# Optimization experiments

Measured on AMD Instinct MI355X. Metric: run time of the kernel, lower is better.

## Reference

```python
import jax, jax.numpy as jnp
import numpy as np

E = 1024
H = 16
CH = E // H

def setup_inputs() -> dict:
    key = jax.random.key(0)
    ks = jax.random.split(key, 9)
    s = E ** -0.5
    return {
        'x': jax.random.normal(ks[0], (4, 2048, E), dtype=jnp.float32),
        'Wq': jax.random.normal(ks[1], (E, E), dtype=jnp.float32) * s,
        'bq': jnp.zeros((E,), dtype=jnp.float32),
        'Wk': jax.random.normal(ks[2], (E, E), dtype=jnp.float32) * s,
        'bk': jnp.zeros((E,), dtype=jnp.float32),
        'Wv': jax.random.normal(ks[3], (E, E), dtype=jnp.float32) * s,
        'bv': jnp.zeros((E,), dtype=jnp.float32),
        'Wo': jax.random.normal(ks[4], (E, E), dtype=jnp.float32) * s,
        'bo': jnp.zeros((E,), dtype=jnp.float32),
    }

def _split_heads(t):
    # [..., n, H*ch] -> [..., H, n, ch]
    b, n, e = t.shape
    return t.reshape(b, n, H, CH).transpose(0, 2, 1, 3)

def reference(x, Wq, bq, Wk, bk, Wv, bv, Wo, bo):
    scale = CH ** -0.5
    q = _split_heads(x @ Wq.T + bq)  # [b,H,n,ch]
    k = _split_heads(x @ Wk.T + bk)
    v = _split_heads(x @ Wv.T + bv)
    att = jnp.einsum('bhqc,bhkc->bhqk', q, k) * scale
    att = jax.nn.softmax(att, axis=-1)
    out = jnp.einsum('bhqk,bhkc->bhqc', att, v)  # [b,H,n,ch]
    b, h, n, c = out.shape
    out = out.transpose(0, 2, 1, 3).reshape(b, n, h * c)
    return out @ Wo.T + bo
```

## Files before the change

### kernel.cpp

```cpp
#include <hip/hip_runtime.h>
#include <stdint.h>

#define EMB   1024
#define NHEAD 16
#define CHD   64
#define NB    4
#define SEQ   2048
#define NTOK  (NB * SEQ)
#define KDIM  1024

typedef __attribute__((ext_vector_type(8))) short  bf16x8;
typedef __attribute__((ext_vector_type(4))) short  short4v;
typedef __attribute__((ext_vector_type(4))) float  f32x4;
typedef __attribute__((ext_vector_type(4))) float  float4v;

__device__ __forceinline__ short f2bf(float f) {
    unsigned int u = __float_as_uint(f);
    u += 0x7fffu + ((u >> 16) & 1u);
    return (short)(u >> 16);
}

__device__ __forceinline__ void async16(const short* g, short* l) {
    __builtin_amdgcn_global_load_lds((__attribute__((address_space(1))) void const*)g,
                                     (__attribute__((address_space(3))) void*)l, 16, 0, 0);
}

__global__ __launch_bounds__(256) void cvt_all(const float* __restrict__ x,
                                               const float* __restrict__ Wq,
                                               const float* __restrict__ Wk,
                                               const float* __restrict__ Wv,
                                               const float* __restrict__ Wo,
                                               short* __restrict__ xb,
                                               short* __restrict__ Wqb,
                                               short* __restrict__ Wkb,
                                               short* __restrict__ Wvb,
                                               short* __restrict__ Wob) {
    int bid = blockIdx.x;
    const float* src;
    short* dst;
    int idx;
    if (bid < 8192) {
        src = x; dst = xb; idx = bid * 256 + threadIdx.x;
    } else {
        int w  = (bid - 8192) >> 10;
        int lb = (bid - 8192) & 1023;
        src = (w == 0) ? Wq : (w == 1) ? Wk : (w == 2) ? Wv : Wo;
        dst = (w == 0) ? Wqb : (w == 1) ? Wkb : (w == 2) ? Wvb : Wob;
        idx = lb * 256 + threadIdx.x;
    }
    float4v v = ((const float4v*)src)[idx];
    short4v s;
    s.x = f2bf(v.x); s.y = f2bf(v.y); s.z = f2bf(v.z); s.w = f2bf(v.w);
    ((short4v*)dst)[idx] = s;
}

__device__ __forceinline__ void gemm_core(const short* __restrict__ Atile,
                                          const short* __restrict__ Btile,
                                          short* As, short* Bs, f32x4 acc[4][4]) {
    const int tid  = threadIdx.x;
    const int wave = tid >> 6, lane = tid & 63;
    const int quad = lane >> 4, l16 = lane & 15;
    const int wm = (wave >> 1) * 64, wn = (wave & 1) * 64;
    const int srow = lane >> 2;
    const int scol = (lane & 3) * 8;

    for (int k0 = 0; k0 < KDIM; k0 += 32) {
        __syncthreads();
#pragma unroll
        for (int c = 0; c < 2; ++c) {
            int chunk = wave * 2 + c;
            int row = chunk * 16 + srow;
            async16(Atile + (size_t)row * KDIM + k0 + scol, As + chunk * 512);
            async16(Btile + (size_t)row * KDIM + k0 + scol, Bs + chunk * 512);
        }
        __syncthreads();
        bf16x8 af[4], bfr[4];
#pragma unroll
        for (int i = 0; i < 4; ++i)
            af[i] = *(const bf16x8*)&As[(wm + i * 16 + l16) * 32 + quad * 8];
#pragma unroll
        for (int j = 0; j < 4; ++j)
            bfr[j] = *(const bf16x8*)&Bs[(wn + j * 16 + l16) * 32 + quad * 8];
#pragma unroll
        for (int i = 0; i < 4; ++i)
#pragma unroll
            for (int j = 0; j < 4; ++j)
                acc[i][j] = __builtin_amdgcn_mfma_f32_16x16x32_bf16(af[i], bfr[j], acc[i][j], 0, 0, 0);
    }
}

#define QSCALE 0.1803368801111204f


#define MFMA16(A,B,C) __builtin_amdgcn_mfma_f32_16x16x32_bf16(A,B,C,0,0,0)
#define BARR  { __builtin_amdgcn_s_barrier(); __builtin_amdgcn_sched_barrier(0); }
#define VMC4  asm volatile("s_waitcnt vmcnt(4)" ::: "memory");
#define VMC0  asm volatile("s_waitcnt vmcnt(0)" ::: "memory");
#define PRIO1 __builtin_amdgcn_s_setprio(1);
#define PRIO0 __builtin_amdgcn_s_setprio(0);

#define STAGE_A_(BUF,H,T) { \
    async16(aS0 + (size_t)(H)*131072 + (T)*64, sm + (BUF)*32768 + (H)*8192 + stA); \
    async16(aS1 + (size_t)(H)*131072 + (T)*64, sm + (BUF)*32768 + (H)*8192 + 4096 + stA); }
#define STAGE_B_(BUF,H,T) { \
    async16(bS0 + (size_t)(H)*131072 + (T)*64, sm + (BUF)*32768 + 16384 + (H)*8192 + stA); \
    async16(bS1 + (size_t)(H)*131072 + (T)*64, sm + (BUF)*32768 + 16384 + (H)*8192 + 4096 + stA); }

#define LDB_(BUF) { \
    const short* _pb = sm + (BUF)*32768 + bro; \
    bfr[0][0] = *(const bf16x8*)(_pb + ac0);        bfr[0][1] = *(const bf16x8*)(_pb + ac1); \
    bfr[1][0] = *(const bf16x8*)(_pb + 1024 + ac0); bfr[1][1] = *(const bf16x8*)(_pb + 1024 + ac1); \
    bfr[2][0] = *(const bf16x8*)(_pb + 2048 + ac0); bfr[2][1] = *(const bf16x8*)(_pb + 2048 + ac1); \
    bfr[3][0] = *(const bf16x8*)(_pb + 3072 + ac0); bfr[3][1] = *(const bf16x8*)(_pb + 3072 + ac1); }

#define LDA_(BUF,Q) { \
    const short* _pa = sm + (BUF)*32768 + aro + (Q)*2048; \
    af[0][0] = *(const bf16x8*)(_pa + ac0);        af[0][1] = *(const bf16x8*)(_pa + ac1); \
    af[1][0] = *(const bf16x8*)(_pa + 1024 + ac0); af[1][1] = *(const bf16x8*)(_pa + 1024 + ac1); }

#define MF_(Q) { \
    acc[2*(Q)][0]   = MFMA16(af[0][0], bfr[0][0], acc[2*(Q)][0]); \
    acc[2*(Q)][0]   = MFMA16(af[0][1], bfr[0][1], acc[2*(Q)][0]); \
    acc[2*(Q)][1]   = MFMA16(af[0][0], bfr[1][0], acc[2*(Q)][1]); \
    acc[2*(Q)][1]   = MFMA16(af[0][1], bfr[1][1], acc[2*(Q)][1]); \
    acc[2*(Q)][2]   = MFMA16(af[0][0], bfr[2][0], acc[2*(Q)][2]); \
    acc[2*(Q)][2]   = MFMA16(af[0][1], bfr[2][1], acc[2*(Q)][2]); \
    acc[2*(Q)][3]   = MFMA16(af[0][0], bfr[3][0], acc[2*(Q)][3]); \
    acc[2*(Q)][3]   = MFMA16(af[0][1], bfr[3][1], acc[2*(Q)][3]); \
    acc[2*(Q)+1][0] = MFMA16(af[1][0], bfr[0][0], acc[2*(Q)+1][0]); \
    acc[2*(Q)+1][0] = MFMA16(af[1][1], bfr[0][1], acc[2*(Q)+1][0]); \
    acc[2*(Q)+1][1] = MFMA16(af[1][0], bfr[1][0], acc[2*(Q)+1][1]); \
    acc[2*(Q)+1][1] = MFMA16(af[1][1], bfr[1][1], acc[2*(Q)+1][1]); \
    acc[2*(Q)+1][2] = MFMA16(af[1][0], bfr[2][0], acc[2*(Q)+1][2]); \
    acc[2*(Q)+1][2] = MFMA16(af[1][1], bfr[2][1], acc[2*(Q)+1][2]); \
    acc[2*(Q)+1][3] = MFMA16(af[1][0], bfr[3][0], acc[2*(Q)+1][3]); \
    acc[2*(Q)+1][3] = MFMA16(af[1][1], bfr[3][1], acc[2*(Q)+1][3]); }

#define WINDOW(RB, AB, TA, BB, TB) \
    LDB_(RB) LDA_(RB,0) STAGE_A_(AB,0,TA) BARR \
    PRIO1 MF_(0) PRIO0 BARR \
    LDA_(RB,1) STAGE_A_(AB,1,TA) BARR \
    PRIO1 MF_(1) PRIO0 BARR \
    LDA_(RB,2) STAGE_B_(BB,0,TB) BARR \
    PRIO1 MF_(2) PRIO0 BARR \
    LDA_(RB,3) STAGE_B_(BB,1,TB) BARR \
    PRIO1 MF_(3) PRIO0 VMC4 BARR

__global__ __launch_bounds__(512, 2) void qk256(const short* __restrict__ xb,
                                                const short* __restrict__ Wqk,
                                                const float* __restrict__ bq,
                                                const float* __restrict__ bk,
                                                short* __restrict__ Qb,
                                                short* __restrict__ Kb) {
    extern __shared__ short sm[];
    const int bm = blockIdx.x, bn = blockIdx.y;
    const int tid = threadIdx.x;
    const int w = tid >> 6, lane = tid & 63;
    const int kq = lane >> 4, l16 = lane & 15;
    const int wmi = w >> 2, wni = w & 3;

    const int colsw = ((lane & 7) * 8) ^ (((lane >> 5) & 1) << 4);
    const short* aS0 = xb  + (size_t)(bm * 256 + w * 8 + (lane >> 3)) * 1024 + colsw;
    const short* aS1 = aS0 + (size_t)64 * 1024;
    const short* bS0 = Wqk + (size_t)(bn * 256 + w * 8 + (lane >> 3)) * 1024 + colsw;
    const short* bS1 = bS0 + (size_t)64 * 1024;
    const int stA = w * 512;

    const int swz = (l16 & 4) ? 16 : 0;
    const int ac0 = (kq * 8) ^ swz;
    const int ac1 = (32 + kq * 8) ^ swz;
    const int aro = wmi * 8192 + l16 * 64;
    const int bro = 16384 + (wni >> 1) * 8192 + ((wni & 1) * 64 + l16) * 64;

    f32x4 acc[8][4];
    const f32x4 z = {0.f, 0.f, 0.f, 0.f};
#pragma unroll
    for (int m = 0; m < 8; ++m)
#pragma unroll
        for (int n = 0; n < 4; ++n) acc[m][n] = z;
    bf16x8 bfr[4][2], af[2][2];

    STAGE_A_(0,0,0) STAGE_A_(0,1,0) STAGE_B_(0,0,0) STAGE_B_(0,1,0)
    STAGE_B_(1,0,1) STAGE_B_(1,1,1)
    VMC4 BARR

    for (int it = 0; it < 7; ++it) {
        const int te = 2 * it;
        WINDOW(0, 1, te + 1, 0, te + 2)
        WINDOW(1, 0, te + 2, 1, te + 3)
    }
    LDB_(0) LDA_(0,0) STAGE_A_(1,0,15) BARR
    PRIO1 MF_(0) PRIO0 BARR
    LDA_(0,1) STAGE_A_(1,1,15) BARR
    PRIO1 MF_(1) PRIO0 BARR
    LDA_(0,2) BARR
    PRIO1 MF_(2) PRIO0 BARR
    LDA_(0,3) BARR
    PRIO1 MF_(3) PRIO0 VMC0 BARR
    LDB_(1)
    LDA_(1,0) MF_(0)
    LDA_(1,1) MF_(1)
    LDA_(1,2) MF_(2)
    LDA_(1,3) MF_(3)

    const bool isQ = (bn < 4);
    const float* bias = isQ ? bq : bk;
    short* dst = isQ ? Qb : Kb;
    const float sc = isQ ? QSCALE : 1.0f;
    const int fb = (bn & 3) * 256 + wni * 64 + l16;
    const int tok0 = bm * 256 + wmi * 128 + kq * 4;
#pragma unroll
    for (int n = 0; n < 4; ++n) {
        const int e = fb + n * 16;
        const int hh = e >> 6, cc = e & 63;
        const float bv_ = bias[e];
#pragma unroll
        for (int m = 0; m < 8; ++m)
#pragma unroll
            for (int r = 0; r < 4; ++r) {
                const int tok = tok0 + m * 16 + r;
                const int bb = tok >> 11, nn = tok & 2047;
                dst[(((size_t)bb * NHEAD + hh) * SEQ + nn) * CHD + cc] =
                    f2bf((acc[m][n][r] + bv_) * sc);
            }
    }
}

__global__ __launch_bounds__(256) void vproj(const short* __restrict__ xb,
                                             const short* __restrict__ Wvb,
                                             const float* __restrict__ bv,
                                             short* __restrict__ Vtb) {
    __shared__ short As[128 * 32], Bs[128 * 32];
    const int bm = blockIdx.x;
    const int ew = blockIdx.y * 128;

    f32x4 acc[4][4];
    const f32x4 z = {0.f, 0.f, 0.f, 0.f};
#pragma unroll
    for (int i = 0; i < 4; ++i)
#pragma unroll
        for (int j = 0; j < 4; ++j) acc[i][j] = z;

    gemm_core(Wvb + (size_t)ew * KDIM, xb + (size_t)bm * 128 * KDIM, As, Bs, acc);

    const int lane = threadIdx.x & 63, wave = threadIdx.x >> 6;
    const int quad = lane >> 4, l16 = lane & 15;
    const int wm = (wave >> 1) * 64, wn = (wave & 1) * 64;
#pragma unroll
    for (int i = 0; i < 4; ++i)
#pragma unroll
        for (int j = 0; j < 4; ++j)
#pragma unroll
            for (int r = 0; r < 4; ++r) {
                int e = ew + wm + i * 16 + quad * 4 + r;
                int token = bm * 128 + wn + j * 16 + l16;
                int bb = token >> 11, nn = token & 2047;
                int hh = e >> 6, cc = e & 63;
                Vtb[(((size_t)bb * NHEAD + hh) * CHD + cc) * SEQ + nn] =
                    f2bf(acc[i][j][r] + bv[e]);
            }
}

__global__ __launch_bounds__(256, 4) void attn(const short* __restrict__ Qb,
                                               const short* __restrict__ Kb,
                                               const short* __restrict__ Vtb,
                                               short* __restrict__ AOb) {
    __shared__ short Ks[16 * 512];
    __shared__ short Vs[16 * 512];

    const int qt = blockIdx.x;
    const int bh = blockIdx.y;
    const int tid = threadIdx.x, wave = tid >> 6, lane = tid & 63;
    const int quad = lane >> 4, l16 = lane & 15;

    const short* Kg = Kb  + (size_t)bh * SEQ * CHD;
    const short* Vg = Vtb + (size_t)bh * CHD * SEQ;

    bf16x8 qf0[2], qf1[2];
#pragma unroll
    for (int g = 0; g < 2; ++g) {
        const short* Qg = Qb + ((size_t)bh * SEQ + qt * 128 + wave * 32 + g * 16 + l16) * CHD;
        qf0[g] = *(const bf16x8*)(Qg + quad * 8);
        qf1[g] = *(const bf16x8*)(Qg + 32 + quad * 8);
    }

    const int kr = lane >> 3, ku = (lane & 7) ^ kr;
    const int vr = lane >> 4, vu = (lane & 15) ^ (vr << 2);

    int koff[4], voff[4];
#pragma unroll
    for (int cc = 0; cc < 4; ++cc) {
        int c = wave * 4 + cc;
        int l = c * 8 + kr;
        int j = l >> 4, m = l & 15;
        int kvg = ((j >> 1) << 5) + ((m >> 2) << 3) + ((j & 1) << 2) + (m & 3);
        koff[cc] = kvg * CHD + ku * 8;
        voff[cc] = (c * 4 + vr) * SEQ + vu * 8;
    }

    const int krow = l16 & 7;
    const int kbase = ((l16 >> 3) * 512) + krow * 64;
    const short* kp0 = Ks + kbase + ((quad ^ krow) << 3);
    const short* kp1 = Ks + kbase + (((4 + quad) ^ krow) << 3);
    const int vrow = l16 & 3;
    const short* vp = Vs + (l16 >> 2) * 512 + vrow * 128 + quad * 8;

    const f32x4 zf = {0.f, 0.f, 0.f, 0.f};
    const bf16x8 onesv = {16256, 16256, 16256, 16256, 16256, 16256, 16256, 16256};
    f32x4 O[2][4];
#pragma unroll
    for (int g = 0; g < 2; ++g)
#pragma unroll
        for (int nb = 0; nb < 4; ++nb) O[g][nb] = zf;
    f32x4 lacc[2];
    lacc[0] = zf; lacc[1] = zf;

    const short* Kgp = Kg;
    const short* Vgp = Vg;

    for (int kt = 0; kt < 16; ++kt) {
        __syncthreads();
#pragma unroll
        for (int cc = 0; cc < 4; ++cc) {
            int c = wave * 4 + cc;
            async16(Kgp + koff[cc], Ks + c * 512);
            async16(Vgp + voff[cc], Vs + c * 512);
        }
        Kgp += 128 * CHD;
        Vgp += 128;
        __syncthreads();

#pragma unroll
        for (int kk = 0; kk < 4; ++kk) {
            bf16x8 kA0 = *(const bf16x8*)(kp0 + (2 * kk) * 1024);
            bf16x8 kA1 = *(const bf16x8*)(kp1 + (2 * kk) * 1024);
            bf16x8 kB0 = *(const bf16x8*)(kp0 + (2 * kk + 1) * 1024);
            bf16x8 kB1 = *(const bf16x8*)(kp1 + (2 * kk + 1) * 1024);

            union { int i[4]; bf16x8 v; } pf[2];
#pragma unroll
            for (int g = 0; g < 2; ++g) {
                f32x4 sA = __builtin_amdgcn_mfma_f32_16x16x32_bf16(kA0, qf0[g], zf, 0, 0, 0);
                sA = __builtin_amdgcn_mfma_f32_16x16x32_bf16(kA1, qf1[g], sA, 0, 0, 0);
                f32x4 sB = __builtin_amdgcn_mfma_f32_16x16x32_bf16(kB0, qf0[g], zf, 0, 0, 0);
                sB = __builtin_amdgcn_mfma_f32_16x16x32_bf16(kB1, qf1[g], sB, 0, 0, 0);

                unsigned a0 = __float_as_uint(__builtin_amdgcn_exp2f(sA.x));
                unsigned a1 = __float_as_uint(__builtin_amdgcn_exp2f(sA.y));
                unsigned a2 = __float_as_uint(__builtin_amdgcn_exp2f(sA.z));
                unsigned a3 = __float_as_uint(__builtin_amdgcn_exp2f(sA.w));
                unsigned b0 = __float_as_uint(__builtin_amdgcn_exp2f(sB.x));
                unsigned b1 = __float_as_uint(__builtin_amdgcn_exp2f(sB.y));
                unsigned b2 = __float_as_uint(__builtin_amdgcn_exp2f(sB.z));
                unsigned b3 = __float_as_uint(__builtin_amdgcn_exp2f(sB.w));
                pf[g].i[0] = __builtin_amdgcn_perm(a1, a0, 0x07060302u);
                pf[g].i[1] = __builtin_amdgcn_perm(a3, a2, 0x07060302u);
                pf[g].i[2] = __builtin_amdgcn_perm(b1, b0, 0x07060302u);
                pf[g].i[3] = __builtin_amdgcn_perm(b3, b2, 0x07060302u);

                lacc[g] = __builtin_amdgcn_mfma_f32_16x16x32_bf16(pf[g].v, onesv, lacc[g], 0, 0, 0);
            }

            const short* vpk = vp + ((kk ^ vrow) << 5);
#pragma unroll
            for (int nb = 0; nb < 4; ++nb) {
                bf16x8 vf = *(const bf16x8*)(vpk + nb * 2048);
#pragma unroll
                for (int g = 0; g < 2; ++g)
                    O[g][nb] = __builtin_amdgcn_mfma_f32_16x16x32_bf16(pf[g].v, vf, O[g][nb], 0, 0, 0);
            }
        }
    }

    const int b = bh >> 4, h = bh & 15;
#pragma unroll
    for (int g = 0; g < 2; ++g) {
        float linv[4];
#pragma unroll
        for (int r = 0; r < 4; ++r) linv[r] = 1.0f / lacc[g][r];
#pragma unroll
        for (int nb = 0; nb < 4; ++nb)
#pragma unroll
            for (int r = 0; r < 4; ++r) {
                int n = qt * 128 + wave * 32 + g * 16 + quad * 4 + r;
                int cc = nb * 16 + l16;
                AOb[((size_t)b * SEQ + n) * EMB + h * CHD + cc] = f2bf(O[g][nb][r] * linv[r]);
            }
    }
}

__global__ __launch_bounds__(256) void out_gemm(const short* __restrict__ AOb,
                                                const short* __restrict__ Wob,
                                                const float* __restrict__ bo,
                                                float* __restrict__ out) {
    __shared__ short As[128 * 32], Bs[128 * 32];
    const int bm = blockIdx.x, bn = blockIdx.y;

    f32x4 acc[4][4];
    const f32x4 z = {0.f, 0.f, 0.f, 0.f};
#pragma unroll
    for (int i = 0; i < 4; ++i)
#pragma unroll
        for (int j = 0; j < 4; ++j) acc[i][j] = z;

    gemm_core(AOb + (size_t)bm * 128 * KDIM, Wob + (size_t)bn * 128 * KDIM, As, Bs, acc);

    const int lane = threadIdx.x & 63, wave = threadIdx.x >> 6;
    const int quad = lane >> 4, l16 = lane & 15;
    const int wm = (wave >> 1) * 64, wn = (wave & 1) * 64;
#pragma unroll
    for (int i = 0; i < 4; ++i)
#pragma unroll
        for (int j = 0; j < 4; ++j)
#pragma unroll
            for (int r = 0; r < 4; ++r) {
                int token = bm * 128 + wm + i * 16 + quad * 4 + r;
                int e = bn * 128 + wn + j * 16 + l16;
                out[(size_t)token * EMB + e] = acc[i][j][r] + bo[e];
            }
}

extern "C" void kernel_launch(void* const* d_in, const int* in_sizes, int n_in,
                              void* d_out, int out_size, void* d_ws, size_t ws_size,
                              hipStream_t stream) {
    const float* x  = (const float*)d_in[0];
    const float* Wq = (const float*)d_in[1];
    const float* bq = (const float*)d_in[2];
    const float* Wk = (const float*)d_in[3];
    const float* bk = (const float*)d_in[4];
    const float* Wv = (const float*)d_in[5];
    const float* bv = (const float*)d_in[6];
    const float* Wo = (const float*)d_in[7];
    const float* bo = (const float*)d_in[8];

    char* ws = (char*)d_ws;
    short* xb  = (short*)(ws + 0);
    short* Wqb = (short*)(ws + (size_t)16 * 1024 * 1024);
    short* Wkb = (short*)(ws + (size_t)18 * 1024 * 1024);
    short* Wvb = (short*)(ws + (size_t)20 * 1024 * 1024);
    short* Wob = (short*)(ws + (size_t)22 * 1024 * 1024);
    short* Qb  = (short*)(ws + (size_t)24 * 1024 * 1024);
    short* Kb  = (short*)(ws + (size_t)40 * 1024 * 1024);
    short* Vtb = (short*)(ws + (size_t)56 * 1024 * 1024);
    short* AOb = (short*)(ws + (size_t)72 * 1024 * 1024);

    static bool s_cfg = false;
    if (!s_cfg) {
        hipFuncSetAttribute(reinterpret_cast<const void*>(qk256),
                            hipFuncAttributeMaxDynamicSharedMemorySize, 131072);
        s_cfg = true;
    }

    cvt_all<<<dim3(8192 + 4096), dim3(256), 0, stream>>>(x, Wq, Wk, Wv, Wo,
                                                         xb, Wqb, Wkb, Wvb, Wob);
    qk256<<<dim3(32, 8), dim3(512), 131072, stream>>>(xb, Wqb, bq, bk, Qb, Kb);
    vproj<<<dim3(64, 8), dim3(256), 0, stream>>>(xb, Wvb, bv, Vtb);
    attn<<<dim3(16, 64), dim3(256), 0, stream>>>(Qb, Kb, Vtb, AOb);
    out_gemm<<<dim3(64, 8), dim3(256), 0, stream>>>(AOb, Wob, bo, (float*)d_out);
}
```

Before: 262.3 us.

## Prefetch K/V tiles into registers to overlap global loads with attention compute

The attention loop no longer issues async global-to-LDS copies between two barriers at the start of each iteration. K/V tiles are now loaded into registers one tile ahead, then written to LDS after the compute for the current tile, so global latency can hide behind the MFMA work. S_setprio is also raised around the MFMA groups. The cost is extra VGPRs for the staging registers and explicit lgkmcnt waits, which may lower occupancy.

```diff
diff --git a/kernel.cpp b/kernel.cpp
--- a/kernel.cpp
+++ b/kernel.cpp
@@ -13,6 +13,7 @@
 typedef __attribute__((ext_vector_type(4))) short  short4v;
 typedef __attribute__((ext_vector_type(4))) float  f32x4;
 typedef __attribute__((ext_vector_type(4))) float  float4v;
+typedef __attribute__((ext_vector_type(4))) int    i32x4;
 
 __device__ __forceinline__ short f2bf(float f) {
     unsigned int u = __float_as_uint(f);
@@ -23,6 +24,10 @@
 __device__ __forceinline__ void async16(const short* g, short* l) {
     __builtin_amdgcn_global_load_lds((__attribute__((address_space(1))) void const*)g,
                                      (__attribute__((address_space(3))) void*)l, 16, 0, 0);
+}
+
+__device__ __forceinline__ i32x4 gload16(const short* g) {
+    return *(const __attribute__((address_space(1))) i32x4*)g;
 }
 
 __global__ __launch_bounds__(256) void cvt_all(const float* __restrict__ x,
@@ -96,6 +101,7 @@
 #define BARR  { __builtin_amdgcn_s_barrier(); __builtin_amdgcn_sched_barrier(0); }
 #define VMC4  asm volatile("s_waitcnt vmcnt(4)" ::: "memory");
 #define VMC0  asm volatile("s_waitcnt vmcnt(0)" ::: "memory");
+#define LGKM0 asm volatile("s_waitcnt lgkmcnt(0)" ::: "memory");
 #define PRIO1 __builtin_amdgcn_s_setprio(1);
 #define PRIO0 __builtin_amdgcn_s_setprio(0);
 
@@ -297,6 +303,8 @@
         koff[cc] = kvg * CHD + ku * 8;
         voff[cc] = (c * 4 + vr) * SEQ + vu * 8;
     }
+    short* wK = Ks + wave * 2048 + lane * 8;
+    short* wV = Vs + wave * 2048 + lane * 8;
 
     const int krow = l16 & 7;
     const int kbase = ((l16 >> 3) * 512) + krow * 64;
@@ -317,19 +325,28 @@
 
     const short* Kgp = Kg;
     const short* Vgp = Vg;
+    i32x4 kreg[4], vreg[4];
+
+#pragma unroll
+    for (int cc = 0; cc < 4; ++cc) {
+        kreg[cc] = gload16(Kgp + koff[cc]);
+        vreg[cc] = gload16(Vgp + voff[cc]);
+    }
+    Kgp += 128 * CHD; Vgp += 128;
+#pragma unroll
+    for (int cc = 0; cc < 4; ++cc) {
+        *(i32x4*)(wK + cc * 512) = kreg[cc];
+        *(i32x4*)(wV + cc * 512) = vreg[cc];
+    }
+#pragma unroll
+    for (int cc = 0; cc < 4; ++cc) {
+        kreg[cc] = gload16(Kgp + koff[cc]);
+        vreg[cc] = gload16(Vgp + voff[cc]);
+    }
+    Kgp += 128 * CHD; Vgp += 128;
+    LGKM0 BARR
 
     for (int kt = 0; kt < 16; ++kt) {
-        __syncthreads();
-#pragma unroll
-        for (int cc = 0; cc < 4; ++cc) {
-            int c = wave * 4 + cc;
-            async16(Kgp + koff[cc], Ks + c * 512);
-            async16(Vgp + voff[cc], Vs + c * 512);
-        }
-        Kgp += 128 * CHD;
-        Vgp += 128;
-        __syncthreads();
-
 #pragma unroll
         for (int kk = 0; kk < 4; ++kk) {
             bf16x8 kA0 = *(const bf16x8*)(kp0 + (2 * kk) * 1024);
@@ -340,10 +357,12 @@
             union { int i[4]; bf16x8 v; } pf[2];
 #pragma unroll
             for (int g = 0; g < 2; ++g) {
+                PRIO1
                 f32x4 sA = __builtin_amdgcn_mfma_f32_16x16x32_bf16(kA0, qf0[g], zf, 0, 0, 0);
                 sA = __builtin_amdgcn_mfma_f32_16x16x32_bf16(kA1, qf1[g], sA, 0, 0, 0);
                 f32x4 sB = __builtin_amdgcn_mfma_f32_16x16x32_bf16(kB0, qf0[g], zf, 0, 0, 0);
                 sB = __builtin_amdgcn_mfma_f32_16x16x32_bf16(kB1, qf1[g], sB, 0, 0, 0);
+                PRIO0
 
                 unsigned a0 = __float_as_uint(__builtin_amdgcn_exp2f(sA.x));
                 unsigned a1 = __float_as_uint(__builtin_amdgcn_exp2f(sA.y));
@@ -362,6 +381,7 @@
             }
 
             const short* vpk = vp + ((kk ^ vrow) << 5);
+            PRIO1
 #pragma unroll
             for (int nb = 0; nb < 4; ++nb) {
                 bf16x8 vf = *(const bf16x8*)(vpk + nb * 2048);
@@ -369,6 +389,30 @@
                 for (int g = 0; g < 2; ++g)
                     O[g][nb] = __builtin_amdgcn_mfma_f32_16x16x32_bf16(pf[g].v, vf, O[g][nb], 0, 0, 0);
             }
+            PRIO0
+        }
+
+        __builtin_amdgcn_sched_barrier(0);
+        __builtin_amdgcn_s_barrier();
+        __builtin_amdgcn_sched_barrier(0);
+        if (kt < 15) {
+#pragma unroll
+            for (int cc = 0; cc < 4; ++cc) {
+                *(i32x4*)(wK + cc * 512) = kreg[cc];
+                *(i32x4*)(wV + cc * 512) = vreg[cc];
+            }
+            if (kt < 14) {
+#pragma unroll
+                for (int cc = 0; cc < 4; ++cc) {
+                    kreg[cc] = gload16(Kgp + koff[cc]);
+                    vreg[cc] = gload16(Vgp + voff[cc]);
+                }
+                Kgp += 128 * CHD; Vgp += 128;
+            }
+            LGKM0
+            __builtin_amdgcn_sched_barrier(0);
+            __builtin_amdgcn_s_barrier();
+            __builtin_amdgcn_sched_barrier(0);
         }
     }
 
```

After: 276.8 us. 1.06x slower.

## Overlap K/V tile loads with split S and PV phases in attention

Applied to the files above, without the earlier changes.

The attention loop is split into a score phase and a PV phase. The next K tile now loads while PV runs, and the next V tile loads while the following score phase runs. MFMA sections get raised wave priority, and the grid becomes 1D with a remapping so blocks sharing a (batch, head) are placed to improve L2 reuse of K/V. The exp'd probabilities for a whole tile are held in registers, which raises register pressure. The schedule also depends on macros (PRIO, VMC, BARR, MFMA16) that are assumed to be defined elsewhere.

```diff
diff --git a/kernel.cpp b/kernel.cpp
--- a/kernel.cpp
+++ b/kernel.cpp
@@ -268,8 +268,10 @@
     __shared__ short Ks[16 * 512];
     __shared__ short Vs[16 * 512];
 
-    const int qt = blockIdx.x;
-    const int bh = blockIdx.y;
+    const int lid = blockIdx.x;
+    const int bh = (lid & 7) * 8 + (lid >> 7);
+    const int qt = (lid >> 3) & 15;
+
     const int tid = threadIdx.x, wave = tid >> 6, lane = tid & 63;
     const int quad = lane >> 4, l16 = lane & 15;
 
@@ -315,61 +317,84 @@
     f32x4 lacc[2];
     lacc[0] = zf; lacc[1] = zf;
 
-    const short* Kgp = Kg;
-    const short* Vgp = Vg;
-
-    for (int kt = 0; kt < 16; ++kt) {
-        __syncthreads();
-#pragma unroll
-        for (int cc = 0; cc < 4; ++cc) {
-            int c = wave * 4 + cc;
-            async16(Kgp + koff[cc], Ks + c * 512);
-            async16(Vgp + voff[cc], Vs + c * 512);
-        }
-        Kgp += 128 * CHD;
-        Vgp += 128;
-        __syncthreads();
-
-#pragma unroll
-        for (int kk = 0; kk < 4; ++kk) {
-            bf16x8 kA0 = *(const bf16x8*)(kp0 + (2 * kk) * 1024);
-            bf16x8 kA1 = *(const bf16x8*)(kp1 + (2 * kk) * 1024);
-            bf16x8 kB0 = *(const bf16x8*)(kp0 + (2 * kk + 1) * 1024);
-            bf16x8 kB1 = *(const bf16x8*)(kp1 + (2 * kk + 1) * 1024);
-
-            union { int i[4]; bf16x8 v; } pf[2];
-#pragma unroll
-            for (int g = 0; g < 2; ++g) {
-                f32x4 sA = __builtin_amdgcn_mfma_f32_16x16x32_bf16(kA0, qf0[g], zf, 0, 0, 0);
-                sA = __builtin_amdgcn_mfma_f32_16x16x32_bf16(kA1, qf1[g], sA, 0, 0, 0);
-                f32x4 sB = __builtin_amdgcn_mfma_f32_16x16x32_bf16(kB0, qf0[g], zf, 0, 0, 0);
-                sB = __builtin_amdgcn_mfma_f32_16x16x32_bf16(kB1, qf1[g], sB, 0, 0, 0);
-
-                unsigned a0 = __float_as_uint(__builtin_amdgcn_exp2f(sA.x));
-                unsigned a1 = __float_as_uint(__builtin_amdgcn_exp2f(sA.y));
-                unsigned a2 = __float_as_uint(__builtin_amdgcn_exp2f(sA.z));
-                unsigned a3 = __float_as_uint(__builtin_amdgcn_exp2f(sA.w));
-                unsigned b0 = __float_as_uint(__builtin_amdgcn_exp2f(sB.x));
-                unsigned b1 = __float_as_uint(__builtin_amdgcn_exp2f(sB.y));
-                unsigned b2 = __float_as_uint(__builtin_amdgcn_exp2f(sB.z));
-                unsigned b3 = __float_as_uint(__builtin_amdgcn_exp2f(sB.w));
-                pf[g].i[0] = __builtin_amdgcn_perm(a1, a0, 0x07060302u);
-                pf[g].i[1] = __builtin_amdgcn_perm(a3, a2, 0x07060302u);
-                pf[g].i[2] = __builtin_amdgcn_perm(b1, b0, 0x07060302u);
-                pf[g].i[3] = __builtin_amdgcn_perm(b3, b2, 0x07060302u);
-
-                lacc[g] = __builtin_amdgcn_mfma_f32_16x16x32_bf16(pf[g].v, onesv, lacc[g], 0, 0, 0);
-            }
-
-            const short* vpk = vp + ((kk ^ vrow) << 5);
-#pragma unroll
-            for (int nb = 0; nb < 4; ++nb) {
-                bf16x8 vf = *(const bf16x8*)(vpk + nb * 2048);
-#pragma unroll
-                for (int g = 0; g < 2; ++g)
-                    O[g][nb] = __builtin_amdgcn_mfma_f32_16x16x32_bf16(pf[g].v, vf, O[g][nb], 0, 0, 0);
-            }
-        }
+#define ATTN_STAGE_K(T) { \
+    const short* _kg = Kg + (size_t)(T) * (128 * CHD); \
+    _Pragma("unroll") \
+    for (int cc = 0; cc < 4; ++cc) \
+        async16(_kg + koff[cc], Ks + (wave * 4 + cc) * 512); }
+#define ATTN_STAGE_V(T) { \
+    const short* _vg = Vg + (size_t)(T) * 128; \
+    _Pragma("unroll") \
+    for (int cc = 0; cc < 4; ++cc) \
+        async16(_vg + voff[cc], Vs + (wave * 4 + cc) * 512); }
+
+#define ATTN_SPHASE { \
+    _Pragma("unroll") \
+    for (int kk = 0; kk < 4; ++kk) { \
+        bf16x8 kA0 = *(const bf16x8*)(kp0 + (2 * kk) * 1024); \
+        bf16x8 kA1 = *(const bf16x8*)(kp1 + (2 * kk) * 1024); \
+        bf16x8 kB0 = *(const bf16x8*)(kp0 + (2 * kk + 1) * 1024); \
+        bf16x8 kB1 = *(const bf16x8*)(kp1 + (2 * kk + 1) * 1024); \
+        _Pragma("unroll") \
+        for (int g = 0; g < 2; ++g) { \
+            PRIO1 \
+            f32x4 sA = MFMA16(kA0, qf0[g], zf); \
+            sA = MFMA16(kA1, qf1[g], sA); \
+            f32x4 sB = MFMA16(kB0, qf0[g], zf); \
+            sB = MFMA16(kB1, qf1[g], sB); \
+            PRIO0 \
+            unsigned a0 = __float_as_uint(__builtin_amdgcn_exp2f(sA.x)); \
+            unsigned a1 = __float_as_uint(__builtin_amdgcn_exp2f(sA.y)); \
+            unsigned a2 = __float_as_uint(__builtin_amdgcn_exp2f(sA.z)); \
+            unsigned a3 = __float_as_uint(__builtin_amdgcn_exp2f(sA.w)); \
+            unsigned b0 = __float_as_uint(__builtin_amdgcn_exp2f(sB.x)); \
+            unsigned b1 = __float_as_uint(__builtin_amdgcn_exp2f(sB.y)); \
+            unsigned b2 = __float_as_uint(__builtin_amdgcn_exp2f(sB.z)); \
+            unsigned b3 = __float_as_uint(__builtin_amdgcn_exp2f(sB.w)); \
+            pf[kk][g].i[0] = __builtin_amdgcn_perm(a1, a0, 0x07060302u); \
+            pf[kk][g].i[1] = __builtin_amdgcn_perm(a3, a2, 0x07060302u); \
+            pf[kk][g].i[2] = __builtin_amdgcn_perm(b1, b0, 0x07060302u); \
+            pf[kk][g].i[3] = __builtin_amdgcn_perm(b3, b2, 0x07060302u); \
+            lacc[g] = MFMA16(pf[kk][g].v, onesv, lacc[g]); \
+        } \
+    } }
+
+#define ATTN_PVPHASE { \
+    _Pragma("unroll") \
+    for (int kk = 0; kk < 4; ++kk) { \
+        const short* vpk = vp + ((kk ^ vrow) << 5); \
+        PRIO1 \
+        _Pragma("unroll") \
+        for (int nb = 0; nb < 4; ++nb) { \
+            bf16x8 vf = *(const bf16x8*)(vpk + nb * 2048); \
+            _Pragma("unroll") \
+            for (int g = 0; g < 2; ++g) \
+                O[g][nb] = MFMA16(pf[kk][g].v, vf, O[g][nb]); \
+        } \
+        PRIO0 \
+    } }
+
+    ATTN_STAGE_K(0) ATTN_STAGE_V(0)
+    VMC4 BARR
+
+    for (int kt = 0; kt < 15; ++kt) {
+        union { int i[4]; bf16x8 v; } pf[4][2];
+        ATTN_SPHASE
+        BARR
+        ATTN_STAGE_K(kt + 1)
+        VMC4
+        BARR
+        ATTN_PVPHASE
+        BARR
+        ATTN_STAGE_V(kt + 1)
+        VMC4
+        BARR
+    }
+    {
+        union { int i[4]; bf16x8 v; } pf[4][2];
+        ATTN_SPHASE
+        VMC0 BARR
+        ATTN_PVPHASE
     }
 
     const int b = bh >> 4, h = bh & 15;
@@ -387,6 +412,10 @@
                 AOb[((size_t)b * SEQ + n) * EMB + h * CHD + cc] = f2bf(O[g][nb][r] * linv[r]);
             }
     }
+#undef ATTN_STAGE_K
+#undef ATTN_STAGE_V
+#undef ATTN_SPHASE
+#undef ATTN_PVPHASE
 }
 
 __global__ __launch_bounds__(256) void out_gemm(const short* __restrict__ AOb,
@@ -455,6 +484,6 @@
                                                          xb, Wqb, Wkb, Wvb, Wob);
     qk256<<<dim3(32, 8), dim3(512), 131072, stream>>>(xb, Wqb, bq, bk, Qb, Kb);
     vproj<<<dim3(64, 8), dim3(256), 0, stream>>>(xb, Wvb, bv, Vtb);
-    attn<<<dim3(16, 64), dim3(256), 0, stream>>>(Qb, Kb, Vtb, AOb);
+    attn<<<dim3(1024), dim3(256), 0, stream>>>(Qb, Kb, Vtb, AOb);
     out_gemm<<<dim3(64, 8), dim3(256), 0, stream>>>(AOb, Wob, bo, (float*)d_out);
 }
```

Result: slower. 275.0 us (+4.8%).

## Fuse V projection into 256-tile QK GEMM, remap attention grid, add MFMA priority

Applied to the files above, without the earlier changes.

The separate 128-tile V projection kernel is folded into the 256x256 QK projection kernel as four extra column blocks. For these blocks the operands are swapped (Wv as A, x as B), so the output comes out already transposed for the Vt layout. This drops one launch and puts V on the more efficient larger-tile pipeline. The attention grid becomes a flat 1D index that interleaves batch-heads across consecutive blocks, likely to spread K/V traffic across caches or XCDs. The MFMA sections in attention are also wrapped in s_setprio raises, at the cost of possible scheduling side effects.

```diff
diff --git a/kernel.cpp b/kernel.cpp
--- a/kernel.cpp
+++ b/kernel.cpp
@@ -146,33 +146,11 @@
     LDA_(RB,3) STAGE_B_(BB,1,TB) BARR \
     PRIO1 MF_(3) PRIO0 VMC4 BARR
 
-__global__ __launch_bounds__(512, 2) void qk256(const short* __restrict__ xb,
-                                                const short* __restrict__ Wqk,
-                                                const float* __restrict__ bq,
-                                                const float* __restrict__ bk,
-                                                short* __restrict__ Qb,
-                                                short* __restrict__ Kb) {
-    extern __shared__ short sm[];
-    const int bm = blockIdx.x, bn = blockIdx.y;
-    const int tid = threadIdx.x;
-    const int w = tid >> 6, lane = tid & 63;
-    const int kq = lane >> 4, l16 = lane & 15;
-    const int wmi = w >> 2, wni = w & 3;
-
-    const int colsw = ((lane & 7) * 8) ^ (((lane >> 5) & 1) << 4);
-    const short* aS0 = xb  + (size_t)(bm * 256 + w * 8 + (lane >> 3)) * 1024 + colsw;
-    const short* aS1 = aS0 + (size_t)64 * 1024;
-    const short* bS0 = Wqk + (size_t)(bn * 256 + w * 8 + (lane >> 3)) * 1024 + colsw;
-    const short* bS1 = bS0 + (size_t)64 * 1024;
-    const int stA = w * 512;
-
-    const int swz = (l16 & 4) ? 16 : 0;
-    const int ac0 = (kq * 8) ^ swz;
-    const int ac1 = (32 + kq * 8) ^ swz;
-    const int aro = wmi * 8192 + l16 * 64;
-    const int bro = 16384 + (wni >> 1) * 8192 + ((wni & 1) * 64 + l16) * 64;
-
-    f32x4 acc[8][4];
+__device__ __forceinline__ void gemm256_core(short* sm,
+        const short* aS0, const short* aS1,
+        const short* bS0, const short* bS1,
+        const int stA, const int ac0, const int ac1,
+        const int aro, const int bro, f32x4 acc[8][4]) {
     const f32x4 z = {0.f, 0.f, 0.f, 0.f};
 #pragma unroll
     for (int m = 0; m < 8; ++m)
@@ -202,63 +180,90 @@
     LDA_(1,1) MF_(1)
     LDA_(1,2) MF_(2)
     LDA_(1,3) MF_(3)
-
-    const bool isQ = (bn < 4);
-    const float* bias = isQ ? bq : bk;
-    short* dst = isQ ? Qb : Kb;
-    const float sc = isQ ? QSCALE : 1.0f;
-    const int fb = (bn & 3) * 256 + wni * 64 + l16;
-    const int tok0 = bm * 256 + wmi * 128 + kq * 4;
-#pragma unroll
-    for (int n = 0; n < 4; ++n) {
-        const int e = fb + n * 16;
-        const int hh = e >> 6, cc = e & 63;
-        const float bv_ = bias[e];
-#pragma unroll
-        for (int m = 0; m < 8; ++m)
-#pragma unroll
-            for (int r = 0; r < 4; ++r) {
-                const int tok = tok0 + m * 16 + r;
-                const int bb = tok >> 11, nn = tok & 2047;
-                dst[(((size_t)bb * NHEAD + hh) * SEQ + nn) * CHD + cc] =
-                    f2bf((acc[m][n][r] + bv_) * sc);
-            }
-    }
-}
-
-__global__ __launch_bounds__(256) void vproj(const short* __restrict__ xb,
-                                             const short* __restrict__ Wvb,
-                                             const float* __restrict__ bv,
-                                             short* __restrict__ Vtb) {
-    __shared__ short As[128 * 32], Bs[128 * 32];
-    const int bm = blockIdx.x;
-    const int ew = blockIdx.y * 128;
-
-    f32x4 acc[4][4];
-    const f32x4 z = {0.f, 0.f, 0.f, 0.f};
-#pragma unroll
-    for (int i = 0; i < 4; ++i)
-#pragma unroll
-        for (int j = 0; j < 4; ++j) acc[i][j] = z;
-
-    gemm_core(Wvb + (size_t)ew * KDIM, xb + (size_t)bm * 128 * KDIM, As, Bs, acc);
-
-    const int lane = threadIdx.x & 63, wave = threadIdx.x >> 6;
-    const int quad = lane >> 4, l16 = lane & 15;
-    const int wm = (wave >> 1) * 64, wn = (wave & 1) * 64;
-#pragma unroll
-    for (int i = 0; i < 4; ++i)
-#pragma unroll
-        for (int j = 0; j < 4; ++j)
-#pragma unroll
-            for (int r = 0; r < 4; ++r) {
-                int e = ew + wm + i * 16 + quad * 4 + r;
-                int token = bm * 128 + wn + j * 16 + l16;
-                int bb = token >> 11, nn = token & 2047;
-                int hh = e >> 6, cc = e & 63;
-                Vtb[(((size_t)bb * NHEAD + hh) * CHD + cc) * SEQ + nn] =
-                    f2bf(acc[i][j][r] + bv[e]);
-            }
+}
+
+__global__ __launch_bounds__(512, 2) void qkv256(const short* __restrict__ xb,
+                                                 const short* __restrict__ Wqk,
+                                                 const short* __restrict__ Wvb,
+                                                 const float* __restrict__ bq,
+                                                 const float* __restrict__ bk,
+                                                 const float* __restrict__ bv,
+                                                 short* __restrict__ Qb,
+                                                 short* __restrict__ Kb,
+                                                 short* __restrict__ Vtb) {
+    extern __shared__ short sm[];
+    const int bm = blockIdx.x, bn = blockIdx.y;
+    const int which = bn >> 2;
+    const int tid = threadIdx.x;
+    const int w = tid >> 6, lane = tid & 63;
+    const int kq = lane >> 4, l16 = lane & 15;
+    const int wmi = w >> 2, wni = w & 3;
+
+    const int colsw = ((lane & 7) * 8) ^ (((lane >> 5) & 1) << 4);
+    const short* Amat;
+    const short* Bmat;
+    if (which == 2) {
+        Amat = Wvb + (size_t)(bn & 3) * 256 * 1024;
+        Bmat = xb  + (size_t)bm * 256 * 1024;
+    } else {
+        Amat = xb  + (size_t)bm * 256 * 1024;
+        Bmat = Wqk + (size_t)bn * 256 * 1024;
+    }
+    const short* aS0 = Amat + (size_t)(w * 8 + (lane >> 3)) * 1024 + colsw;
+    const short* aS1 = aS0 + (size_t)64 * 1024;
+    const short* bS0 = Bmat + (size_t)(w * 8 + (lane >> 3)) * 1024 + colsw;
+    const short* bS1 = bS0 + (size_t)64 * 1024;
+    const int stA = w * 512;
+
+    const int swz = (l16 & 4) ? 16 : 0;
+    const int ac0 = (kq * 8) ^ swz;
+    const int ac1 = (32 + kq * 8) ^ swz;
+    const int aro = wmi * 8192 + l16 * 64;
+    const int bro = 16384 + (wni >> 1) * 8192 + ((wni & 1) * 64 + l16) * 64;
+
+    f32x4 acc[8][4];
+    gemm256_core(sm, aS0, aS1, bS0, bS1, stA, ac0, ac1, aro, bro, acc);
+
+    if (which == 2) {
+        const int f0 = (bn & 3) * 256 + wmi * 128 + kq * 4;
+        const int t0 = bm * 256 + wni * 64 + l16;
+#pragma unroll
+        for (int n = 0; n < 4; ++n) {
+            const int tok = t0 + n * 16;
+            const int bb = tok >> 11, nn = tok & 2047;
+#pragma unroll
+            for (int m = 0; m < 8; ++m)
+#pragma unroll
+                for (int r = 0; r < 4; ++r) {
+                    const int e = f0 + m * 16 + r;
+                    const int hh = e >> 6, cc = e & 63;
+                    Vtb[(((size_t)bb * NHEAD + hh) * CHD + cc) * SEQ + nn] =
+                        f2bf(acc[m][n][r] + bv[e]);
+                }
+        }
+    } else {
+        const bool isQ = (which == 0);
+        const float* bias = isQ ? bq : bk;
+        short* dst = isQ ? Qb : Kb;
+        const float sc = isQ ? QSCALE : 1.0f;
+        const int fb = (bn & 3) * 256 + wni * 64 + l16;
+        const int tok0 = bm * 256 + wmi * 128 + kq * 4;
+#pragma unroll
+        for (int n = 0; n < 4; ++n) {
+            const int e = fb + n * 16;
+            const int hh = e >> 6, cc = e & 63;
+            const float bv_ = bias[e];
+#pragma unroll
+            for (int m = 0; m < 8; ++m)
+#pragma unroll
+                for (int r = 0; r < 4; ++r) {
+                    const int tok = tok0 + m * 16 + r;
+                    const int bb = tok >> 11, nn = tok & 2047;
+                    dst[(((size_t)bb * NHEAD + hh) * SEQ + nn) * CHD + cc] =
+                        f2bf((acc[m][n][r] + bv_) * sc);
+                }
+        }
+    }
 }
 
 __global__ __launch_bounds__(256, 4) void attn(const short* __restrict__ Qb,
@@ -268,8 +273,10 @@
     __shared__ short Ks[16 * 512];
     __shared__ short Vs[16 * 512];
 
-    const int qt = blockIdx.x;
-    const int bh = blockIdx.y;
+    const int lid = blockIdx.x;
+    const int bh = (lid & 7) * 8 + (lid >> 7);
+    const int qt = (lid >> 3) & 15;
+
     const int tid = threadIdx.x, wave = tid >> 6, lane = tid & 63;
     const int quad = lane >> 4, l16 = lane & 15;
 
@@ -340,10 +347,12 @@
             union { int i[4]; bf16x8 v; } pf[2];
 #pragma unroll
             for (int g = 0; g < 2; ++g) {
+                PRIO1
                 f32x4 sA = __builtin_amdgcn_mfma_f32_16x16x32_bf16(kA0, qf0[g], zf, 0, 0, 0);
                 sA = __builtin_amdgcn_mfma_f32_16x16x32_bf16(kA1, qf1[g], sA, 0, 0, 0);
                 f32x4 sB = __builtin_amdgcn_mfma_f32_16x16x32_bf16(kB0, qf0[g], zf, 0, 0, 0);
                 sB = __builtin_amdgcn_mfma_f32_16x16x32_bf16(kB1, qf1[g], sB, 0, 0, 0);
+                PRIO0
 
                 unsigned a0 = __float_as_uint(__builtin_amdgcn_exp2f(sA.x));
                 unsigned a1 = __float_as_uint(__builtin_amdgcn_exp2f(sA.y));
@@ -362,6 +371,7 @@
             }
 
             const short* vpk = vp + ((kk ^ vrow) << 5);
+            PRIO1
 #pragma unroll
             for (int nb = 0; nb < 4; ++nb) {
                 bf16x8 vf = *(const bf16x8*)(vpk + nb * 2048);
@@ -369,6 +379,7 @@
                 for (int g = 0; g < 2; ++g)
                     O[g][nb] = __builtin_amdgcn_mfma_f32_16x16x32_bf16(pf[g].v, vf, O[g][nb], 0, 0, 0);
             }
+            PRIO0
         }
     }
 
@@ -446,15 +457,14 @@
 
     static bool s_cfg = false;
     if (!s_cfg) {
-        hipFuncSetAttribute(reinterpret_cast<const void*>(qk256),
+        hipFuncSetAttribute(reinterpret_cast<const void*>(qkv256),
                             hipFuncAttributeMaxDynamicSharedMemorySize, 131072);
         s_cfg = true;
     }
 
     cvt_all<<<dim3(8192 + 4096), dim3(256), 0, stream>>>(x, Wq, Wk, Wv, Wo,
                                                          xb, Wqb, Wkb, Wvb, Wob);
-    qk256<<<dim3(32, 8), dim3(512), 131072, stream>>>(xb, Wqb, bq, bk, Qb, Kb);
-    vproj<<<dim3(64, 8), dim3(256), 0, stream>>>(xb, Wvb, bv, Vtb);
-    attn<<<dim3(16, 64), dim3(256), 0, stream>>>(Qb, Kb, Vtb, AOb);
+    qkv256<<<dim3(32, 12), dim3(512), 131072, stream>>>(xb, Wqb, Wvb, bq, bk, bv, Qb, Kb, Vtb);
+    attn<<<dim3(1024), dim3(256), 0, stream>>>(Qb, Kb, Vtb, AOb);
     out_gemm<<<dim3(64, 8), dim3(256), 0, stream>>>(AOb, Wob, bo, (float*)d_out);
 }
```

After: 276.1 us. +5.3%, slower.
